# Performance work log

Hardware: AMD Instinct MI355X
Metric: run time of the kernel (lower is better)

Reference implementation:

```python
import jax, jax.numpy as jnp
import numpy as np

B, N, K = 4, 50000, 128   # batch, surface points, deformation nodes
GD = 128                  # SDF grid resolution (D=H=W)


def setup_inputs() -> dict:
    key = jax.random.key(0)
    ks = jax.random.split(key, 7)
    constants = jax.random.normal(ks[0], (B, K), dtype=jnp.float32)
    scales = 0.05 + 0.25 * jax.random.uniform(ks[1], (B, K), dtype=jnp.float32)
    # proper-ish rotations via QR of random matrices
    M = jax.random.normal(ks[2], (B, K, 3, 3), dtype=jnp.float32)
    rotations, _ = jnp.linalg.qr(M)
    centers = jax.random.uniform(ks[3], (B, K, 3), dtype=jnp.float32, minval=-0.5, maxval=0.5)
    surface_samples = jax.random.uniform(ks[4], (B, N, 6), dtype=jnp.float32, minval=-0.5, maxval=0.5)
    grid = jax.random.normal(ks[5], (B, GD, GD, GD), dtype=jnp.float32)
    # world2grid maps world [-0.5,0.5] -> grid index [0, GD-1]
    w2g = np.zeros((B, 4, 4), dtype=np.float32)
    w2g[:, 0, 0] = w2g[:, 1, 1] = w2g[:, 2, 2] = float(GD - 1)
    w2g[:, :3, 3] = float(GD - 1) / 2.0
    w2g[:, 3, 3] = 1.0
    world2grid = jnp.asarray(w2g)
    return {"constants": constants, "scales": scales, "rotations": rotations,
            "centers": centers, "surface_samples": surface_samples,
            "grid": grid, "world2grid": world2grid}


def _trilinear_border(vol, xyz):
    """torch grid_sample (5D, bilinear, align_corners=True, border) for one batch.
    vol: (D,H,W); xyz: (N,3) normalized coords in [-1,1], order (x,y,z)."""
    D, H, W = vol.shape
    x = jnp.clip((xyz[:, 0] + 1.0) * 0.5 * (W - 1), 0.0, W - 1)
    y = jnp.clip((xyz[:, 1] + 1.0) * 0.5 * (H - 1), 0.0, H - 1)
    z = jnp.clip((xyz[:, 2] + 1.0) * 0.5 * (D - 1), 0.0, D - 1)
    x0 = jnp.floor(x); y0 = jnp.floor(y); z0 = jnp.floor(z)
    fx = x - x0; fy = y - y0; fz = z - z0
    x0i = x0.astype(jnp.int32); x1i = jnp.minimum(x0i + 1, W - 1)
    y0i = y0.astype(jnp.int32); y1i = jnp.minimum(y0i + 1, H - 1)
    z0i = z0.astype(jnp.int32); z1i = jnp.minimum(z0i + 1, D - 1)
    c000 = vol[z0i, y0i, x0i]; c001 = vol[z0i, y0i, x1i]
    c010 = vol[z0i, y1i, x0i]; c011 = vol[z0i, y1i, x1i]
    c100 = vol[z1i, y0i, x0i]; c101 = vol[z1i, y0i, x1i]
    c110 = vol[z1i, y1i, x0i]; c111 = vol[z1i, y1i, x1i]
    c00 = c000 * (1 - fx) + c001 * fx
    c01 = c010 * (1 - fx) + c011 * fx
    c10 = c100 * (1 - fx) + c101 * fx
    c11 = c110 * (1 - fx) + c111 * fx
    c0 = c00 * (1 - fy) + c01 * fy
    c1 = c10 * (1 - fy) + c11 * fy
    return c0 * (1 - fz) + c1 * fz


def reference(constants, scales, rotations, centers, surface_samples, grid, world2grid):
    pts = surface_samples[..., :3]                       # (B,N,3)
    diff = pts[:, :, None, :] - centers[:, None, :, :]   # (B,N,K,3)  == p - t_source
    d2 = jnp.sum(diff * diff, axis=-1)                   # (B,N,K)
    # sample_rbf_weights with use_constants=True
    w = jnp.exp(-d2 / (2.0 * scales * scales)[:, None, :]) * (constants * constants)[:, None, :]
    w = w / jnp.sum(w, axis=-1, keepdims=True)           # normalize over nodes

    # target = roll batch by -1 (source_idx+1 mod B)
    R_t = jnp.roll(rotations, -1, axis=0)
    R_rel = jnp.einsum('bkij,bklj->bkil', R_t, rotations)       # R_target @ R_source^T
    c_t = jnp.roll(centers, -1, axis=0)
    transformed = jnp.einsum('bkij,bnkj->bnki', R_rel, diff) + c_t[:, None, :, :]
    blended = jnp.einsum('bnk,bnki->bni', w, transformed)        # (B,N,3)

    w2g_t = jnp.roll(world2grid, -1, axis=0)
    A = w2g_t[:, :3, :3]
    t = w2g_t[:, :3, 3]
    gcs = jnp.einsum('bij,bnj->bni', A, blended) + t[:, None, :]  # grid coords (x,y,z)

    D, H, W = grid.shape[1], grid.shape[2], grid.shape[3]
    denom = jnp.array([W - 1, H - 1, D - 1], dtype=gcs.dtype)
    gcs = 2.0 * (gcs / denom) - 1.0                               # normalize to [-1,1]

    grid_t = jnp.roll(grid, -1, axis=0)
    sdf = jax.vmap(_trilinear_border)(grid_t, gcs)                # (B,N)
    return jnp.sum(jnp.mean(sdf * sdf, axis=1))
```

## Files before the change

kernel.cpp:

```cpp
#include <hip/hip_runtime.h>
#include <stdint.h>

#define K_   128
#define GD_  128
#define PSTR 20
#define KPW  32
#define J_   8
#define PPB  (64 * J_)

static __device__ __forceinline__ float fast_exp2(float x) {
#if __has_builtin(__builtin_amdgcn_exp2f)
    return __builtin_amdgcn_exp2f(x);
#else
    return exp2f(x);
#endif
}

__global__ void surf_param_kernel(
    const float* __restrict__ constants,
    const float* __restrict__ scales,
    const float* __restrict__ rotations,
    const float* __restrict__ centers,
    const float* __restrict__ w2g,
    float* __restrict__ params,
    float* __restrict__ out,
    int B)
{
    int idx = blockIdx.x * blockDim.x + threadIdx.x;
    if (idx == 0) out[0] = 0.0f;
    if (idx >= B * K_) return;
    int b = idx / K_, k = idx - b * K_;
    int bn = (b + 1 == B) ? 0 : (b + 1);
    const float L2E = 1.4426950408889634f;

    const float* R  = rotations + (size_t)(b  * K_ + k) * 9;
    const float* Rt = rotations + (size_t)(bn * K_ + k) * 9;
    float m[9];
#pragma unroll
    for (int i = 0; i < 3; ++i)
#pragma unroll
        for (int l = 0; l < 3; ++l)
            m[i * 3 + l] = Rt[i * 3 + 0] * R[l * 3 + 0]
                         + Rt[i * 3 + 1] * R[l * 3 + 1]
                         + Rt[i * 3 + 2] * R[l * 3 + 2];

    const float* Aw = w2g + (size_t)bn * 16;
    float G[9], A[9] = {Aw[0], Aw[1], Aw[2], Aw[4], Aw[5], Aw[6], Aw[8], Aw[9], Aw[10]};
    float T[3] = {Aw[3], Aw[7], Aw[11]};
#pragma unroll
    for (int i = 0; i < 3; ++i)
#pragma unroll
        for (int l = 0; l < 3; ++l)
            G[i * 3 + l] = A[i * 3 + 0] * m[0 * 3 + l]
                         + A[i * 3 + 1] * m[1 * 3 + l]
                         + A[i * 3 + 2] * m[2 * 3 + l];

    const float* c  = centers + (size_t)(b  * K_ + k) * 3;
    const float* ct = centers + (size_t)(bn * K_ + k) * 3;
    float c0 = c[0], c1 = c[1], c2 = c[2];
    float vw0 = ct[0] - (m[0] * c0 + m[1] * c1 + m[2] * c2);
    float vw1 = ct[1] - (m[3] * c0 + m[4] * c1 + m[5] * c2);
    float vw2 = ct[2] - (m[6] * c0 + m[7] * c1 + m[8] * c2);
    float v0 = A[0] * vw0 + A[1] * vw1 + A[2] * vw2 + T[0];
    float v1 = A[3] * vw0 + A[4] * vw1 + A[5] * vw2 + T[1];
    float v2 = A[6] * vw0 + A[7] * vw1 + A[8] * vw2 + T[2];

    float sig = scales[b * K_ + k];
    float s   = 1.0f / (2.0f * sig * sig);
    float con = constants[b * K_ + k];
    float s2n = -s * L2E;
    float r   = log2f(con * con) + s2n * (c0 * c0 + c1 * c1 + c2 * c2);

    float* o = params + (size_t)idx * PSTR;
    o[0] = G[0]; o[1] = G[1]; o[2] = G[2]; o[3] = G[3];
    o[4] = G[4]; o[5] = G[5]; o[6] = G[6]; o[7] = G[7];
    o[8] = G[8]; o[9] = v0;  o[10] = v1;  o[11] = v2;
    o[12] = -2.0f * s2n * c0;
    o[13] = -2.0f * s2n * c1;
    o[14] = -2.0f * s2n * c2;
    o[15] = r;
    o[16] = s2n;
    o[17] = 0.f; o[18] = 0.f; o[19] = 0.f;
}

__global__ __launch_bounds__(256, 2) void surf_loss_kernel(
    const float* __restrict__ sp,
    const float* __restrict__ grid,
    const float* __restrict__ params,
    float* __restrict__ out,
    int N, int B, int bpb)
{
    __shared__ float4 lds_part[4 * J_ * 64];
    __shared__ float  red[4];

    const int tid  = threadIdx.x;
    const int lane = tid & 63;
    const int wave = tid >> 6;
    const int blk  = blockIdx.x;
    const int b    = blk / bpb;
    const int base = (blk - b * bpb) * PPB;
    const int bn   = (b + 1 == B) ? 0 : (b + 1);

    float px[J_], py[J_], pz[J_], pq[J_];
    float ax[J_], ay[J_], az[J_], aw[J_];
    const float* spb = sp + (size_t)b * N * 6;
#pragma unroll
    for (int j = 0; j < J_; ++j) {
        int n = base + (j << 6) + lane;
        int nn = (n < N) ? n : 0;
        const float* q = spb + (size_t)nn * 6;
        px[j] = q[0]; py[j] = q[1]; pz[j] = q[2];
        pq[j] = px[j] * px[j] + py[j] * py[j] + pz[j] * pz[j];
        ax[j] = 0.f; ay[j] = 0.f; az[j] = 0.f; aw[j] = 0.f;
    }

    const float4* Pv = (const float4*)(params
                     + ((size_t)b * K_ + (size_t)wave * KPW) * PSTR);
#pragma unroll 2
    for (int kk = 0; kk < KPW; ++kk) {
        const float4 f0 = Pv[kk * 5 + 0];
        const float4 f1 = Pv[kk * 5 + 1];
        const float4 f2 = Pv[kk * 5 + 2];
        const float4 f3 = Pv[kk * 5 + 3];
        const float  s2 = Pv[kk * 5 + 4].x;
#pragma unroll
        for (int j = 0; j < J_; ++j) {
            float e = f3.w + f3.x * px[j] + f3.y * py[j] + f3.z * pz[j] + s2 * pq[j];
            float w = fast_exp2(e);
            float tx = f2.y + f0.x * px[j] + f0.y * py[j] + f0.z * pz[j];
            float ty = f2.z + f0.w * px[j] + f1.x * py[j] + f1.y * pz[j];
            float tz = f2.w + f1.z * px[j] + f1.w * py[j] + f2.x * pz[j];
            ax[j] += w * tx;
            ay[j] += w * ty;
            az[j] += w * tz;
            aw[j] += w;
        }
    }

#pragma unroll
    for (int j = 0; j < J_; ++j)
        lds_part[((wave * J_ + j) << 6) + lane] = make_float4(ax[j], ay[j], az[j], aw[j]);
    __syncthreads();

    float accum = 0.0f;
    const float* gb = grid + (size_t)bn * GD_ * GD_ * GD_;
#pragma unroll
    for (int e2 = 0; e2 < 2; ++e2) {
        int pi = (e2 << 8) + tid;
        int j  = pi >> 6, ln = pi & 63;
        float sx = 0.f, sy = 0.f, sz = 0.f, sw = 0.f;
#pragma unroll
        for (int w = 0; w < 4; ++w) {
            float4 t = lds_part[((w * J_ + j) << 6) + ln];
            sx += t.x; sy += t.y; sz += t.z; sw += t.w;
        }
        int n = base + pi;
        if (n < N) {
            float inv = 1.0f / sw;
            float x = fminf(fmaxf(sx * inv, 0.0f), (float)(GD_ - 1));
            float y = fminf(fmaxf(sy * inv, 0.0f), (float)(GD_ - 1));
            float z = fminf(fmaxf(sz * inv, 0.0f), (float)(GD_ - 1));
            float x0f = floorf(x), y0f = floorf(y), z0f = floorf(z);
            float fx = x - x0f, fy = y - y0f, fz = z - z0f;
            int x0 = (int)x0f, y0 = (int)y0f, z0 = (int)z0f;
            int x1 = x0 + 1 > GD_ - 1 ? GD_ - 1 : x0 + 1;
            int y1 = y0 + 1 > GD_ - 1 ? GD_ - 1 : y0 + 1;
            int z1 = z0 + 1 > GD_ - 1 ? GD_ - 1 : z0 + 1;
            int zy00 = (z0 * GD_ + y0) * GD_;
            int zy01 = (z0 * GD_ + y1) * GD_;
            int zy10 = (z1 * GD_ + y0) * GD_;
            int zy11 = (z1 * GD_ + y1) * GD_;
            float c000 = gb[zy00 + x0], c001 = gb[zy00 + x1];
            float c010 = gb[zy01 + x0], c011 = gb[zy01 + x1];
            float c100 = gb[zy10 + x0], c101 = gb[zy10 + x1];
            float c110 = gb[zy11 + x0], c111 = gb[zy11 + x1];
            float ofx = 1.0f - fx, ofy = 1.0f - fy, ofz = 1.0f - fz;
            float c00 = c000 * ofx + c001 * fx;
            float c01 = c010 * ofx + c011 * fx;
            float c10 = c100 * ofx + c101 * fx;
            float c11 = c110 * ofx + c111 * fx;
            float c0 = c00 * ofy + c01 * fy;
            float c1 = c10 * ofy + c11 * fy;
            float sdf = c0 * ofz + c1 * fz;
            accum += sdf * sdf;
        }
    }

#pragma unroll
    for (int off = 32; off > 0; off >>= 1)
        accum += __shfl_down(accum, off, 64);
    if (lane == 0) red[wave] = accum;
    __syncthreads();
    if (tid == 0)
        atomicAdd(out, (red[0] + red[1] + red[2] + red[3]) * (1.0f / (float)N));
}

extern "C" void kernel_launch(void* const* d_in, const int* in_sizes, int n_in,
                              void* d_out, int out_size, void* d_ws, size_t ws_size,
                              hipStream_t stream) {
    const float* constants = (const float*)d_in[0];
    const float* scales    = (const float*)d_in[1];
    const float* rotations = (const float*)d_in[2];
    const float* centers   = (const float*)d_in[3];
    const float* sp        = (const float*)d_in[4];
    const float* grid      = (const float*)d_in[5];
    const float* w2g       = (const float*)d_in[6];
    float* out = (float*)d_out;
    float* params = (float*)d_ws;

    const int B = in_sizes[6] / 16;
    const int N = in_sizes[4] / (6 * B);

    int np = B * K_;
    hipLaunchKernelGGL(surf_param_kernel, dim3((np + 255) / 256), dim3(256), 0, stream,
                       constants, scales, rotations, centers, w2g, params, out, B);

    const int bpb = (N + PPB - 1) / PPB;
    hipLaunchKernelGGL(surf_loss_kernel, dim3(B * bpb), dim3(256), 0, stream,
                       sp, grid, params, out, N, B, bpb);
}
```

Before: 118.7 us.

## Split blend and trilinear gather into separate kernels, stage params in LDS

The fused loss kernel becomes two kernels. A blend kernel stages the per-batch node parameters in shared memory and writes un-normalized blended coordinates plus weight sums to a workspace buffer. A separate gather kernel then does the normalization, the trilinear SDF lookup and the reduction, using one thread per point. The goal is to separate the compute-bound exp/blend phase from the latency-bound grid gather so each gets its own occupancy. The cost is an extra launch and a global round trip of one float4 per point.

```diff
diff --git a/kernel.cpp b/kernel.cpp
--- a/kernel.cpp
+++ b/kernel.cpp
@@ -7,6 +7,7 @@
 #define KPW  32
 #define J_   8
 #define PPB  (64 * J_)
+#define PART_OFF 65536
 
 static __device__ __forceinline__ float fast_exp2(float x) {
 #if __has_builtin(__builtin_amdgcn_exp2f)
@@ -83,15 +84,14 @@
     o[17] = 0.f; o[18] = 0.f; o[19] = 0.f;
 }
 
-__global__ __launch_bounds__(256, 2) void surf_loss_kernel(
+__global__ __launch_bounds__(256) void surf_blend_kernel(
     const float* __restrict__ sp,
-    const float* __restrict__ grid,
     const float* __restrict__ params,
-    float* __restrict__ out,
+    float4* __restrict__ part,
     int N, int B, int bpb)
 {
+    __shared__ float  lds_par[K_ * PSTR];
     __shared__ float4 lds_part[4 * J_ * 64];
-    __shared__ float  red[4];
 
     const int tid  = threadIdx.x;
     const int lane = tid & 63;
@@ -99,7 +99,13 @@
     const int blk  = blockIdx.x;
     const int b    = blk / bpb;
     const int base = (blk - b * bpb) * PPB;
-    const int bn   = (b + 1 == B) ? 0 : (b + 1);
+
+    {
+        const float4* Pv = (const float4*)(params + (size_t)b * K_ * PSTR);
+        float4* Lv = (float4*)lds_par;
+        for (int t = tid; t < K_ * PSTR / 4; t += 256)
+            Lv[t] = Pv[t];
+    }
 
     float px[J_], py[J_], pz[J_], pq[J_];
     float ax[J_], ay[J_], az[J_], aw[J_];
@@ -114,15 +120,17 @@
         ax[j] = 0.f; ay[j] = 0.f; az[j] = 0.f; aw[j] = 0.f;
     }
 
-    const float4* Pv = (const float4*)(params
-                     + ((size_t)b * K_ + (size_t)wave * KPW) * PSTR);
+    __syncthreads();
+
+    const int k0 = wave * KPW;
 #pragma unroll 2
     for (int kk = 0; kk < KPW; ++kk) {
-        const float4 f0 = Pv[kk * 5 + 0];
-        const float4 f1 = Pv[kk * 5 + 1];
-        const float4 f2 = Pv[kk * 5 + 2];
-        const float4 f3 = Pv[kk * 5 + 3];
-        const float  s2 = Pv[kk * 5 + 4].x;
+        const float4* f = (const float4*)(lds_par + (k0 + kk) * PSTR);
+        const float4 f0 = f[0];
+        const float4 f1 = f[1];
+        const float4 f2 = f[2];
+        const float4 f3 = f[3];
+        const float  s2 = lds_par[(k0 + kk) * PSTR + 16];
 #pragma unroll
         for (int j = 0; j < J_; ++j) {
             float e = f3.w + f3.x * px[j] + f3.y * py[j] + f3.z * pz[j] + s2 * pq[j];
@@ -142,54 +150,71 @@
         lds_part[((wave * J_ + j) << 6) + lane] = make_float4(ax[j], ay[j], az[j], aw[j]);
     __syncthreads();
 
-    float accum = 0.0f;
-    const float* gb = grid + (size_t)bn * GD_ * GD_ * GD_;
 #pragma unroll
     for (int e2 = 0; e2 < 2; ++e2) {
         int pi = (e2 << 8) + tid;
         int j  = pi >> 6, ln = pi & 63;
-        float sx = 0.f, sy = 0.f, sz = 0.f, sw = 0.f;
+        float4 s = make_float4(0.f, 0.f, 0.f, 0.f);
 #pragma unroll
         for (int w = 0; w < 4; ++w) {
             float4 t = lds_part[((w * J_ + j) << 6) + ln];
-            sx += t.x; sy += t.y; sz += t.z; sw += t.w;
+            s.x += t.x; s.y += t.y; s.z += t.z; s.w += t.w;
         }
         int n = base + pi;
-        if (n < N) {
-            float inv = 1.0f / sw;
-            float x = fminf(fmaxf(sx * inv, 0.0f), (float)(GD_ - 1));
-            float y = fminf(fmaxf(sy * inv, 0.0f), (float)(GD_ - 1));
-            float z = fminf(fmaxf(sz * inv, 0.0f), (float)(GD_ - 1));
-            float x0f = floorf(x), y0f = floorf(y), z0f = floorf(z);
-            float fx = x - x0f, fy = y - y0f, fz = z - z0f;
-            int x0 = (int)x0f, y0 = (int)y0f, z0 = (int)z0f;
-            int x1 = x0 + 1 > GD_ - 1 ? GD_ - 1 : x0 + 1;
-            int y1 = y0 + 1 > GD_ - 1 ? GD_ - 1 : y0 + 1;
-            int z1 = z0 + 1 > GD_ - 1 ? GD_ - 1 : z0 + 1;
-            int zy00 = (z0 * GD_ + y0) * GD_;
-            int zy01 = (z0 * GD_ + y1) * GD_;
-            int zy10 = (z1 * GD_ + y0) * GD_;
-            int zy11 = (z1 * GD_ + y1) * GD_;
-            float c000 = gb[zy00 + x0], c001 = gb[zy00 + x1];
-            float c010 = gb[zy01 + x0], c011 = gb[zy01 + x1];
-            float c100 = gb[zy10 + x0], c101 = gb[zy10 + x1];
-            float c110 = gb[zy11 + x0], c111 = gb[zy11 + x1];
-            float ofx = 1.0f - fx, ofy = 1.0f - fy, ofz = 1.0f - fz;
-            float c00 = c000 * ofx + c001 * fx;
-            float c01 = c010 * ofx + c011 * fx;
-            float c10 = c100 * ofx + c101 * fx;
-            float c11 = c110 * ofx + c111 * fx;
-            float c0 = c00 * ofy + c01 * fy;
-            float c1 = c10 * ofy + c11 * fy;
-            float sdf = c0 * ofz + c1 * fz;
-            accum += sdf * sdf;
-        }
-    }
-
+        if (n < N)
+            part[(size_t)b * N + n] = s;
+    }
+}
+
+__global__ __launch_bounds__(256) void surf_gather_kernel(
+    const float4* __restrict__ part,
+    const float* __restrict__ grid,
+    float* __restrict__ out,
+    int N, int B)
+{
+    const int tid = threadIdx.x;
+    const int idx = blockIdx.x * 256 + tid;
+    float accum = 0.0f;
+    if (idx < B * N) {
+        int b = idx / N, n = idx - b * N;
+        int bn = (b + 1 == B) ? 0 : (b + 1);
+        float4 s = part[idx];
+        float inv = 1.0f / s.w;
+        float x = fminf(fmaxf(s.x * inv, 0.0f), (float)(GD_ - 1));
+        float y = fminf(fmaxf(s.y * inv, 0.0f), (float)(GD_ - 1));
+        float z = fminf(fmaxf(s.z * inv, 0.0f), (float)(GD_ - 1));
+        float x0f = floorf(x), y0f = floorf(y), z0f = floorf(z);
+        float fx = x - x0f, fy = y - y0f, fz = z - z0f;
+        int x0 = (int)x0f, y0 = (int)y0f, z0 = (int)z0f;
+        int x1 = x0 + 1 > GD_ - 1 ? GD_ - 1 : x0 + 1;
+        int y1 = y0 + 1 > GD_ - 1 ? GD_ - 1 : y0 + 1;
+        int z1 = z0 + 1 > GD_ - 1 ? GD_ - 1 : z0 + 1;
+        const float* gb = grid + (size_t)bn * GD_ * GD_ * GD_;
+        int zy00 = (z0 * GD_ + y0) * GD_;
+        int zy01 = (z0 * GD_ + y1) * GD_;
+        int zy10 = (z1 * GD_ + y0) * GD_;
+        int zy11 = (z1 * GD_ + y1) * GD_;
+        float c000 = gb[zy00 + x0], c001 = gb[zy00 + x1];
+        float c010 = gb[zy01 + x0], c011 = gb[zy01 + x1];
+        float c100 = gb[zy10 + x0], c101 = gb[zy10 + x1];
+        float c110 = gb[zy11 + x0], c111 = gb[zy11 + x1];
+        float ofx = 1.0f - fx, ofy = 1.0f - fy, ofz = 1.0f - fz;
+        float c00 = c000 * ofx + c001 * fx;
+        float c01 = c010 * ofx + c011 * fx;
+        float c10 = c100 * ofx + c101 * fx;
+        float c11 = c110 * ofx + c111 * fx;
+        float c0 = c00 * ofy + c01 * fy;
+        float c1 = c10 * ofy + c11 * fy;
+        float sdf = c0 * ofz + c1 * fz;
+        accum = sdf * sdf;
+    }
+
+    __shared__ float red[4];
 #pragma unroll
     for (int off = 32; off > 0; off >>= 1)
         accum += __shfl_down(accum, off, 64);
-    if (lane == 0) red[wave] = accum;
+    int wave = tid >> 6;
+    if ((tid & 63) == 0) red[wave] = accum;
     __syncthreads();
     if (tid == 0)
         atomicAdd(out, (red[0] + red[1] + red[2] + red[3]) * (1.0f / (float)N));
@@ -206,7 +231,8 @@
     const float* grid      = (const float*)d_in[5];
     const float* w2g       = (const float*)d_in[6];
     float* out = (float*)d_out;
-    float* params = (float*)d_ws;
+    float*  params = (float*)d_ws;
+    float4* part   = (float4*)((char*)d_ws + PART_OFF);
 
     const int B = in_sizes[6] / 16;
     const int N = in_sizes[4] / (6 * B);
@@ -216,6 +242,10 @@
                        constants, scales, rotations, centers, w2g, params, out, B);
 
     const int bpb = (N + PPB - 1) / PPB;
-    hipLaunchKernelGGL(surf_loss_kernel, dim3(B * bpb), dim3(256), 0, stream,
-                       sp, grid, params, out, N, B, bpb);
-}
+    hipLaunchKernelGGL(surf_blend_kernel, dim3(B * bpb), dim3(256), 0, stream,
+                       sp, params, part, N, B, bpb);
+
+    const int gblk = (B * N + 255) / 256;
+    hipLaunchKernelGGL(surf_gather_kernel, dim3(gblk), dim3(256), 0, stream,
+                       part, grid, out, N, B);
+}
```

Result: slower. 127.0 us (+6.9%).
